# Performance work log

Measured on AMD Instinct MI355X. Metric: run time of the kernel, lower is better.

The kernel has to match this reference:

```python
import jax, jax.numpy as jnp
import numpy as np

N, F, C1, H, C2, E = 50000, 256, 32, 8, 16, 800000
NEG_SLOPE = 0.2


def gat_layer(x, src, dst, W, a_src, a_dst, b, heads, out_c, concat):
    n = x.shape[0]
    h = (x @ W).reshape(n, heads, out_c)               # [N,H,C]
    al_src = jnp.sum(h * a_src, axis=-1)               # [N,H]
    al_dst = jnp.sum(h * a_dst, axis=-1)               # [N,H]
    e = jax.nn.leaky_relu(al_src[src] + al_dst[dst], NEG_SLOPE)  # [E,H]
    # segment softmax over incoming edges of each dst node
    m = jax.ops.segment_max(e, dst, num_segments=n)
    e = jnp.exp(e - m[dst])
    denom = jax.ops.segment_sum(e, dst, num_segments=n)
    alpha = e / (denom[dst] + 1e-16)                   # [E,H]
    msg = h[src] * alpha[..., None]                    # [E,H,C]
    out = jax.ops.segment_sum(msg, dst, num_segments=n)
    out = out.reshape(n, heads * out_c) if concat else out.mean(axis=1)
    return out + b


def conv1d(x, w, b):
    # x: [1,C,N], w: [O,I,K], 'same' padding (K=5 -> pad 2)
    pad = (w.shape[-1] - 1) // 2
    y = jax.lax.conv_general_dilated(x, w, (1,), [(pad, pad)],
                                     dimension_numbers=('NCH', 'OIH', 'NCH'))
    return y + b[None, :, None]


def setup_inputs() -> dict:
    key = jax.random.key(0)
    ks = jax.random.split(key, 20)
    s = lambda k, shp, sc: jax.random.normal(k, shp, jnp.float32) * sc
    inp = {
        'x': jax.random.normal(ks[0], (N, F), jnp.float32),
        'edge_index': jax.random.randint(ks[1], (2, E), 0, N, jnp.int32),
        'W1': s(ks[2], (F, H * C1), 0.06),
        'a_src1': s(ks[3], (H, C1), 0.1), 'a_dst1': s(ks[4], (H, C1), 0.1),
        'b1': jnp.zeros((H * C1,), jnp.float32),
        'W2': s(ks[5], (H * C1, C2), 0.06),
        'a_src2': s(ks[6], (1, C2), 0.1), 'a_dst2': s(ks[7], (1, C2), 0.1),
        'b2': jnp.zeros((C2,), jnp.float32),
        'proj_w': s(ks[8], (C2, 1), 0.2), 'proj_b': jnp.zeros((1,), jnp.float32),
        'c1_w': s(ks[9], (C2, C2, 5), 0.1), 'c1_b': jnp.zeros((C2,), jnp.float32),
        'c2_w': s(ks[10], (C2, C2, 5), 0.1), 'c2_b': jnp.zeros((C2,), jnp.float32),
        'lin_w': s(ks[11], (2 * C2, C2), 0.15), 'lin_b': jnp.zeros((C2,), jnp.float32),
    }
    return inp


def reference(x, edge_index, W1, a_src1, a_dst1, b1, W2, a_src2, a_dst2, b2,
              proj_w, proj_b, c1_w, c1_b, c2_w, c2_b, lin_w, lin_b):
    n = x.shape[0]
    loops = jnp.arange(n, dtype=edge_index.dtype)
    src = jnp.concatenate([edge_index[0], loops])  # PyG GATConv adds self-loops
    dst = jnp.concatenate([edge_index[1], loops])

    h = jax.nn.relu(gat_layer(x, src, dst, W1, a_src1, a_dst1, b1, H, C1, True))
    x1 = gat_layer(h, src, dst, W2, a_src2, a_dst2, b2, 1, C2, False)  # [N,C2]

    g = (x1 @ proj_w + proj_b)[:, 0]                  # [N]
    sort_idx = jnp.argsort(g)
    inverse_idx = jnp.argsort(sort_idx)
    sorted_x = g[sort_idx][:, None] * x1[sort_idx]    # [N,C2]
    sx = sorted_x.T[None]                             # [1,C2,N]
    sx = jax.nn.relu(conv1d(sx, c1_w, c1_b))
    sx = conv1d(sx, c2_w, c2_b)
    x2 = sx[0].T[inverse_idx]                         # [N,C2]

    out = jnp.concatenate([x1, x2], axis=1) @ lin_w + lin_b
    return jax.nn.log_softmax(out, axis=1)
```

## Files before the change

### kernel.cpp

```cpp
#include <hip/hip_runtime.h>
#include <math.h>

#define NBUCKET 65536

__device__ __forceinline__ float leakyrelu02(float v) { return v > 0.f ? v : 0.2f * v; }

__global__ __launch_bounds__(256) void k_gemm1(const float* __restrict__ A,
                                               const float* __restrict__ B,
                                               float* __restrict__ C, int M) {
  __shared__ float As[16][132];
  __shared__ float Bs[16][68];
  const int m0 = blockIdx.x * 128;
  const int n0 = blockIdx.y * 64;
  const int tid = threadIdx.x;
  const int tm = tid & 15;
  const int tn = tid >> 4;
  float acc[8][4];
#pragma unroll
  for (int i = 0; i < 8; ++i)
#pragma unroll
    for (int j = 0; j < 4; ++j) acc[i][j] = 0.f;

  const int ar = tid & 127, aseg = (tid >> 7) * 8;
  const int br = tid >> 4, bc = (tid & 15) * 4;

  for (int k0 = 0; k0 < 256; k0 += 16) {
    float4 a0 = make_float4(0.f, 0.f, 0.f, 0.f);
    float4 a1 = make_float4(0.f, 0.f, 0.f, 0.f);
    if (m0 + ar < M) {
      const float* ap = A + (size_t)(m0 + ar) * 256 + k0 + aseg;
      a0 = *(const float4*)(ap);
      a1 = *(const float4*)(ap + 4);
    }
    As[aseg + 0][ar] = a0.x;
    As[aseg + 1][ar] = a0.y;
    As[aseg + 2][ar] = a0.z;
    As[aseg + 3][ar] = a0.w;
    As[aseg + 4][ar] = a1.x;
    As[aseg + 5][ar] = a1.y;
    As[aseg + 6][ar] = a1.z;
    As[aseg + 7][ar] = a1.w;
    *(float4*)&Bs[br][bc] = *(const float4*)(B + (size_t)(k0 + br) * 256 + n0 + bc);
    __syncthreads();
#pragma unroll
    for (int kk = 0; kk < 16; ++kk) {
      float a[8], b[4];
      *(float4*)&a[0] = *(const float4*)&As[kk][tm * 4];
      *(float4*)&a[4] = *(const float4*)&As[kk][64 + tm * 4];
      *(float4*)&b[0] = *(const float4*)&Bs[kk][tn * 4];
#pragma unroll
      for (int i = 0; i < 8; ++i)
#pragma unroll
        for (int j = 0; j < 4; ++j) acc[i][j] += a[i] * b[j];
    }
    __syncthreads();
  }
#pragma unroll
  for (int i = 0; i < 8; ++i) {
    int m = m0 + ((i < 4) ? (tm * 4 + i) : (64 + tm * 4 + i - 4));
    if (m < M) {
      float4 o = make_float4(acc[i][0], acc[i][1], acc[i][2], acc[i][3]);
      *(float4*)(C + (size_t)m * 256 + n0 + tn * 4) = o;
    }
  }
}

__global__ __launch_bounds__(256) void k_al1(const float* __restrict__ h_lin,
                                             const float* __restrict__ a_src,
                                             const float* __restrict__ a_dst,
                                             float* __restrict__ als,
                                             float* __restrict__ ald, int N) {
  int gid = blockIdx.x * 256 + threadIdx.x;
  int n = gid >> 6;
  int l = threadIdx.x & 63;
  if (n >= N) return;
  float4 h4 = *(const float4*)(h_lin + (size_t)n * 256 + l * 4);
  float4 vs = *(const float4*)(a_src + l * 4);
  float4 vd = *(const float4*)(a_dst + l * 4);
  float ps = h4.x * vs.x + h4.y * vs.y + h4.z * vs.z + h4.w * vs.w;
  float pd = h4.x * vd.x + h4.y * vd.y + h4.z * vd.z + h4.w * vd.w;
  ps += __shfl_xor(ps, 1); pd += __shfl_xor(pd, 1);
  ps += __shfl_xor(ps, 2); pd += __shfl_xor(pd, 2);
  ps += __shfl_xor(ps, 4); pd += __shfl_xor(pd, 4);
  if ((l & 7) == 0) {
    als[(size_t)n * 8 + (l >> 3)] = ps;
    ald[(size_t)n * 8 + (l >> 3)] = pd;
  }
}

__global__ __launch_bounds__(256) void k_hist(const int* __restrict__ ei,
                                              int* __restrict__ counts, int E, int N) {
  int e = blockIdx.x * 256 + threadIdx.x;
  if (e >= E + N) return;
  int d = (e < E) ? ei[E + e] : (e - E);
  atomicAdd(&counts[d], 1);
}

__global__ __launch_bounds__(1024) void k_scan(const int* __restrict__ counts,
                                               int* __restrict__ offsets,
                                               int* __restrict__ cursor, int chunk) {
  __shared__ int part[1024];
  const int t = threadIdx.x;
  const int base = t * chunk;
  int ssum = 0;
  for (int i = 0; i < chunk; i += 4) {
    int4 v = *(const int4*)(counts + base + i);
    ssum += v.x + v.y + v.z + v.w;
  }
  part[t] = ssum;
  __syncthreads();
  for (int d = 1; d < 1024; d <<= 1) {
    int v = (t >= d) ? part[t - d] : 0;
    __syncthreads();
    part[t] += v;
    __syncthreads();
  }
  int run = (t == 0) ? 0 : part[t - 1];
  for (int i = 0; i < chunk; i += 4) {
    int4 v = *(const int4*)(counts + base + i);
    int4 o;
    o.x = run; run += v.x;
    o.y = run; run += v.y;
    o.z = run; run += v.z;
    o.w = run; run += v.w;
    *(int4*)(offsets + base + i) = o;
    if (cursor) *(int4*)(cursor + base + i) = o;
  }
  if (t == 1023) offsets[1024 * chunk] = run;
}

__global__ __launch_bounds__(256) void k_scatter_ew(
    const int* __restrict__ ei, const float* __restrict__ als1,
    const float* __restrict__ ald1, int* __restrict__ cursor,
    int* __restrict__ csr_src, int* __restrict__ csr_dst,
    float* __restrict__ ew, int E, int N) {
  int e = blockIdx.x * 256 + threadIdx.x;
  if (e >= E + N) return;
  int d, s;
  if (e < E) { d = ei[E + e]; s = ei[e]; }
  else { d = e - E; s = d; }
  int pos = atomicAdd(&cursor[d], 1);
  csr_src[pos] = s;
  csr_dst[pos] = d;
  float4 as0 = *(const float4*)(als1 + (size_t)s * 8);
  float4 as1 = *(const float4*)(als1 + (size_t)s * 8 + 4);
  float4 ad0 = *(const float4*)(ald1 + (size_t)d * 8);
  float4 ad1 = *(const float4*)(ald1 + (size_t)d * 8 + 4);
  float4 w0, w1;
  w0.x = expf(leakyrelu02(as0.x + ad0.x));
  w0.y = expf(leakyrelu02(as0.y + ad0.y));
  w0.z = expf(leakyrelu02(as0.z + ad0.z));
  w0.w = expf(leakyrelu02(as0.w + ad0.w));
  w1.x = expf(leakyrelu02(as1.x + ad1.x));
  w1.y = expf(leakyrelu02(as1.y + ad1.y));
  w1.z = expf(leakyrelu02(as1.z + ad1.z));
  w1.w = expf(leakyrelu02(as1.w + ad1.w));
  *(float4*)(ew + (size_t)pos * 8) = w0;
  *(float4*)(ew + (size_t)pos * 8 + 4) = w1;
}

__global__ __launch_bounds__(256) void k_ew2(const int* __restrict__ csr_src,
                                             const int* __restrict__ csr_dst,
                                             const float* __restrict__ als2,
                                             const float* __restrict__ ald2,
                                             float* __restrict__ ew2, int Etot) {
  int t = blockIdx.x * 256 + threadIdx.x;
  if (t >= Etot) return;
  ew2[t] = expf(leakyrelu02(als2[csr_src[t]] + ald2[csr_dst[t]]));
}

__global__ __launch_bounds__(256) void k_gat1(
    const float* __restrict__ h_lin, const float* __restrict__ ew,
    const float* __restrict__ b1, const int* __restrict__ offsets,
    const int* __restrict__ csr_src, const float* __restrict__ W2,
    const float* __restrict__ a_src2, const float* __restrict__ a_dst2,
    float* __restrict__ h2, float* __restrict__ als2, float* __restrict__ ald2, int N) {
  __shared__ float w2s[4352];
  __shared__ float rowbuf[4][256];
  for (int i = threadIdx.x; i < 4096; i += 256) w2s[(i >> 4) * 17 + (i & 15)] = W2[i];
  __syncthreads();

  const int w = threadIdx.x >> 6;
  const int l = threadIdx.x & 63;
  const int half = l >> 5;
  const int li = l & 31;
  const int h3 = li >> 2;
  const int n = blockIdx.x * 4 + w;
  if (n >= N) return;

  const int off = offsets[n];
  const int deg = offsets[n + 1] - off;
  const float* hb = h_lin + li * 8;

  float c0 = 0.f, c1 = 0.f, c2 = 0.f, c3 = 0.f, c4 = 0.f, c5 = 0.f, c6 = 0.f, c7 = 0.f;
  float sw = 0.f;
  int e = 0;
  for (; e + 8 <= deg; e += 8) {
    const int p0 = off + e + half;
    int s0 = csr_src[p0];
    int s1 = csr_src[p0 + 2];
    int s2 = csr_src[p0 + 4];
    int s3 = csr_src[p0 + 6];
    float w0 = ew[(size_t)p0 * 8 + h3];
    float w1 = ew[(size_t)(p0 + 2) * 8 + h3];
    float w2v = ew[(size_t)(p0 + 4) * 8 + h3];
    float w3 = ew[(size_t)(p0 + 6) * 8 + h3];
    const float* r0p = hb + (size_t)s0 * 256;
    const float* r1p = hb + (size_t)s1 * 256;
    const float* r2p = hb + (size_t)s2 * 256;
    const float* r3p = hb + (size_t)s3 * 256;
    float4 r0a = *(const float4*)(r0p), r0b = *(const float4*)(r0p + 4);
    float4 r1a = *(const float4*)(r1p), r1b = *(const float4*)(r1p + 4);
    float4 r2a = *(const float4*)(r2p), r2b = *(const float4*)(r2p + 4);
    float4 r3a = *(const float4*)(r3p), r3b = *(const float4*)(r3p + 4);
    sw += (w0 + w1) + (w2v + w3);
    c0 += w0 * r0a.x + w1 * r1a.x + w2v * r2a.x + w3 * r3a.x;
    c1 += w0 * r0a.y + w1 * r1a.y + w2v * r2a.y + w3 * r3a.y;
    c2 += w0 * r0a.z + w1 * r1a.z + w2v * r2a.z + w3 * r3a.z;
    c3 += w0 * r0a.w + w1 * r1a.w + w2v * r2a.w + w3 * r3a.w;
    c4 += w0 * r0b.x + w1 * r1b.x + w2v * r2b.x + w3 * r3b.x;
    c5 += w0 * r0b.y + w1 * r1b.y + w2v * r2b.y + w3 * r3b.y;
    c6 += w0 * r0b.z + w1 * r1b.z + w2v * r2b.z + w3 * r3b.z;
    c7 += w0 * r0b.w + w1 * r1b.w + w2v * r2b.w + w3 * r3b.w;
  }
  for (; e < deg; e += 2) {
    int ee = e + half;
    if (ee < deg) {
      int p = off + ee;
      int s = csr_src[p];
      float ww = ew[(size_t)p * 8 + h3];
      const float* rp = hb + (size_t)s * 256;
      float4 ra = *(const float4*)(rp), rb = *(const float4*)(rp + 4);
      sw += ww;
      c0 += ww * ra.x; c1 += ww * ra.y; c2 += ww * ra.z; c3 += ww * ra.w;
      c4 += ww * rb.x; c5 += ww * rb.y; c6 += ww * rb.z; c7 += ww * rb.w;
    }
  }
  c0 += __shfl_xor(c0, 32); c1 += __shfl_xor(c1, 32);
  c2 += __shfl_xor(c2, 32); c3 += __shfl_xor(c3, 32);
  c4 += __shfl_xor(c4, 32); c5 += __shfl_xor(c5, 32);
  c6 += __shfl_xor(c6, 32); c7 += __shfl_xor(c7, 32);
  sw += __shfl_xor(sw, 32);
  const float inv = 1.f / (sw + 1e-16f);

  if (half == 0) {
    float4 ba = *(const float4*)(b1 + li * 8);
    float4 bbv = *(const float4*)(b1 + li * 8 + 4);
    rowbuf[w][li * 8 + 0] = fmaxf(c0 * inv + ba.x, 0.f);
    rowbuf[w][li * 8 + 1] = fmaxf(c1 * inv + ba.y, 0.f);
    rowbuf[w][li * 8 + 2] = fmaxf(c2 * inv + ba.z, 0.f);
    rowbuf[w][li * 8 + 3] = fmaxf(c3 * inv + ba.w, 0.f);
    rowbuf[w][li * 8 + 4] = fmaxf(c4 * inv + bbv.x, 0.f);
    rowbuf[w][li * 8 + 5] = fmaxf(c5 * inv + bbv.y, 0.f);
    rowbuf[w][li * 8 + 6] = fmaxf(c6 * inv + bbv.z, 0.f);
    rowbuf[w][li * 8 + 7] = fmaxf(c7 * inv + bbv.w, 0.f);
  }
  asm volatile("s_waitcnt lgkmcnt(0)" ::: "memory");

  const int o = l & 15;
  const int grp = l >> 4;
  float a2 = 0.f;
#pragma unroll 8
  for (int t = 0; t < 64; ++t) {
    int cc = grp * 64 + ((t + grp * 8) & 63);
    a2 += rowbuf[w][cc] * w2s[cc * 17 + o];
  }
  a2 += __shfl_xor(a2, 16);
  a2 += __shfl_xor(a2, 32);

  if (l < 16) {
    h2[(size_t)n * 16 + l] = a2;
    float ps = a2 * a_src2[l];
    float pd = a2 * a_dst2[l];
    ps += __shfl_xor(ps, 1); pd += __shfl_xor(pd, 1);
    ps += __shfl_xor(ps, 2); pd += __shfl_xor(pd, 2);
    ps += __shfl_xor(ps, 4); pd += __shfl_xor(pd, 4);
    ps += __shfl_xor(ps, 8); pd += __shfl_xor(pd, 8);
    if (l == 0) { als2[n] = ps; ald2[n] = pd; }
  }
}

__global__ __launch_bounds__(256) void k_gat2(
    const float* __restrict__ h2, const float* __restrict__ ew2,
    const float* __restrict__ b2, const float* __restrict__ proj_w,
    const float* __restrict__ proj_b, const int* __restrict__ offsets,
    const int* __restrict__ csr_src, float* __restrict__ x1,
    float* __restrict__ g, unsigned long long* __restrict__ keys,
    int* __restrict__ bhist, int N) {
  const int w = threadIdx.x >> 6;
  const int l = threadIdx.x & 63;
  const int n = blockIdx.x * 4 + w;
  if (n >= N) return;
  const int off = offsets[n];
  const int deg = offsets[n + 1] - off;
  const int slot = l >> 4;
  const int c = l & 15;

  float acc = 0.f, sw = 0.f;
  int e0 = 0;
  for (; e0 + 8 <= deg; e0 += 8) {
    int pA = off + e0 + slot;
    int pB = off + e0 + 4 + slot;
    int sA = csr_src[pA];
    int sB = csr_src[pB];
    float wA = ew2[pA];
    float wB = ew2[pB];
    float hA = h2[(size_t)sA * 16 + c];
    float hB = h2[(size_t)sB * 16 + c];
    sw += wA + wB;
    acc += wA * hA + wB * hB;
  }
  for (; e0 < deg; e0 += 4) {
    int e = e0 + slot;
    if (e < deg) {
      int p = off + e;
      int s = csr_src[p];
      float v = ew2[p];
      sw += v;
      acc += v * h2[(size_t)s * 16 + c];
    }
  }
  acc += __shfl_xor(acc, 16); sw += __shfl_xor(sw, 16);
  acc += __shfl_xor(acc, 32); sw += __shfl_xor(sw, 32);
  float x1v = acc / (sw + 1e-16f) + b2[c];

  float pg = x1v * proj_w[c];
  pg += __shfl_xor(pg, 1);
  pg += __shfl_xor(pg, 2);
  pg += __shfl_xor(pg, 4);
  pg += __shfl_xor(pg, 8);
  if (l < 16) x1[(size_t)n * 16 + l] = x1v;
  if (l == 0) {
    float gv = pg + proj_b[0];
    g[n] = gv;
    unsigned u = __float_as_uint(gv);
    u = (u & 0x80000000u) ? ~u : (u | 0x80000000u);
    keys[n] = (((unsigned long long)u) << 32) | (unsigned)n;
    atomicAdd(&bhist[u >> 16], 1);
  }
}

__global__ __launch_bounds__(256) void k_bscatter(const unsigned long long* __restrict__ keys,
                                                  int* __restrict__ cursor,
                                                  unsigned long long* __restrict__ bkeys, int N) {
  int n = blockIdx.x * 256 + threadIdx.x;
  if (n >= N) return;
  unsigned long long k = keys[n];
  int b = (int)(k >> 48);
  int pos = atomicAdd(&cursor[b], 1);
  bkeys[pos] = k;
}

__global__ __launch_bounds__(256) void k_brank(const unsigned long long* __restrict__ bkeys,
                                               const int* __restrict__ boffs,
                                               const float* __restrict__ g,
                                               const float* __restrict__ x1,
                                               int* __restrict__ rank,
                                               float* __restrict__ sortedv, int N) {
  int pos = blockIdx.x * 256 + threadIdx.x;
  if (pos >= N) return;
  unsigned long long k = bkeys[pos];
  int b = (int)(k >> 48);
  int lo = boffs[b], hi = boffs[b + 1];
  int r = lo;
  for (int j = lo; j < hi; ++j) r += (bkeys[j] < k) ? 1 : 0;
  int idx = (int)(unsigned)(k & 0xffffffffull);
  rank[idx] = r;
  float gv = g[idx];
#pragma unroll
  for (int c = 0; c < 16; c += 4) {
    float4 v = *(const float4*)(x1 + (size_t)idx * 16 + c);
    float4 o = make_float4(gv * v.x, gv * v.y, gv * v.z, gv * v.w);
    *(float4*)(sortedv + (size_t)r * 16 + c) = o;
  }
}

__global__ __launch_bounds__(256) void k_conv(const float* __restrict__ in,
                                              const float* __restrict__ wgt,
                                              const float* __restrict__ bias,
                                              float* __restrict__ out, int N, int relu) {
  __shared__ float s[260][17];
  __shared__ float ws[1280];
  __shared__ float bs[16];
  const int p0 = blockIdx.x * 256;
  for (int i = threadIdx.x; i < 1280; i += 256) ws[i] = wgt[i];
  if (threadIdx.x < 16) bs[threadIdx.x] = bias[threadIdx.x];
  for (int idx = threadIdx.x; idx < 260 * 16; idx += 256) {
    int lp = idx >> 4, c = idx & 15;
    int gp = p0 - 2 + lp;
    s[lp][c] = (gp >= 0 && gp < N) ? in[(size_t)gp * 16 + c] : 0.f;
  }
  __syncthreads();
  const int p = p0 + threadIdx.x;
  if (p >= N) return;
  float acc[16];
#pragma unroll
  for (int o = 0; o < 16; ++o) acc[o] = bs[o];
  for (int k = 0; k < 5; ++k) {
    for (int c = 0; c < 16; ++c) {
      float xv = s[threadIdx.x + k][c];
#pragma unroll
      for (int o = 0; o < 16; ++o) acc[o] += ws[(o * 16 + c) * 5 + k] * xv;
    }
  }
#pragma unroll
  for (int o = 0; o < 16; ++o) {
    float v = acc[o];
    if (relu) v = fmaxf(v, 0.f);
    out[(size_t)p * 16 + o] = v;
  }
}

__global__ __launch_bounds__(256) void k_final(
    const float* __restrict__ x1, const float* __restrict__ c2out,
    const int* __restrict__ rank, const float* __restrict__ lin_w,
    const float* __restrict__ lin_b, float* __restrict__ out, int N) {
  __shared__ float lw[512];
  __shared__ float lb[16];
  for (int i = threadIdx.x; i < 512; i += 256) lw[i] = lin_w[i];
  if (threadIdx.x < 16) lb[threadIdx.x] = lin_b[threadIdx.x];
  __syncthreads();
  const int n = blockIdx.x * 256 + threadIdx.x;
  if (n >= N) return;
  float xa[16], xb[16];
  const int r = rank[n];
#pragma unroll
  for (int c = 0; c < 16; c += 4) {
    float4 va = *(const float4*)(x1 + (size_t)n * 16 + c);
    float4 vb = *(const float4*)(c2out + (size_t)r * 16 + c);
    xa[c] = va.x; xa[c + 1] = va.y; xa[c + 2] = va.z; xa[c + 3] = va.w;
    xb[c] = vb.x; xb[c + 1] = vb.y; xb[c + 2] = vb.z; xb[c + 3] = vb.w;
  }
  float z[16];
#pragma unroll
  for (int o = 0; o < 16; ++o) z[o] = lb[o];
#pragma unroll
  for (int c = 0; c < 16; ++c) {
    float va = xa[c], vb = xb[c];
#pragma unroll
    for (int o = 0; o < 16; ++o) z[o] += va * lw[c * 16 + o] + vb * lw[(16 + c) * 16 + o];
  }
  float m = z[0];
#pragma unroll
  for (int o = 1; o < 16; ++o) m = fmaxf(m, z[o]);
  float ssum = 0.f;
#pragma unroll
  for (int o = 0; o < 16; ++o) ssum += expf(z[o] - m);
  float lse = m + logf(ssum);
#pragma unroll
  for (int o = 0; o < 16; ++o) out[(size_t)n * 16 + o] = z[o] - lse;
}

extern "C" void kernel_launch(void* const* d_in, const int* in_sizes, int n_in,
                              void* d_out, int out_size, void* d_ws, size_t ws_size,
                              hipStream_t stream) {
  const float* x = (const float*)d_in[0];
  const int* ei = (const int*)d_in[1];
  const float* W1 = (const float*)d_in[2];
  const float* a_src1 = (const float*)d_in[3];
  const float* a_dst1 = (const float*)d_in[4];
  const float* b1 = (const float*)d_in[5];
  const float* W2 = (const float*)d_in[6];
  const float* a_src2 = (const float*)d_in[7];
  const float* a_dst2 = (const float*)d_in[8];
  const float* b2 = (const float*)d_in[9];
  const float* proj_w = (const float*)d_in[10];
  const float* proj_b = (const float*)d_in[11];
  const float* c1_w = (const float*)d_in[12];
  const float* c1_b = (const float*)d_in[13];
  const float* c2_w = (const float*)d_in[14];
  const float* c2_b = (const float*)d_in[15];
  const float* lin_w = (const float*)d_in[16];
  const float* lin_b = (const float*)d_in[17];
  float* out = (float*)d_out;

  const int N = in_sizes[0] / 256;
  const int E = in_sizes[1] / 2;
  const int Etot = E + N;

  int chunk = (N + 1023) / 1024;
  chunk = (chunk + 3) & ~3;
  const int Npad = 1024 * chunk;

  char* ws = (char*)d_ws;
  size_t off = 0;
  auto alloc = [&](size_t bytes) -> void* {
    void* p = ws + off;
    off = (off + bytes + 255) & ~(size_t)255;
    return p;
  };
  float* h_lin = (float*)alloc((size_t)N * 256 * 4);
  float* als1 = (float*)alloc((size_t)N * 8 * 4);
  float* ald1 = (float*)alloc((size_t)N * 8 * 4);
  int* counts = (int*)alloc((size_t)Npad * 4);
  int* offsets = (int*)alloc((size_t)(Npad + 1) * 4);
  int* cursor = (int*)alloc((size_t)Npad * 4);
  int* csr_src = (int*)alloc((size_t)Etot * 4);
  int* csr_dst = (int*)alloc((size_t)Etot * 4);
  float* ew = (float*)alloc((size_t)Etot * 8 * 4);
  float* ew2 = (float*)alloc((size_t)Etot * 4);
  float* h2 = (float*)alloc((size_t)N * 16 * 4);
  float* als2 = (float*)alloc((size_t)N * 4);
  float* ald2 = (float*)alloc((size_t)N * 4);
  float* x1 = (float*)alloc((size_t)N * 16 * 4);
  float* gbuf = (float*)alloc((size_t)N * 4);
  unsigned long long* keys = (unsigned long long*)alloc((size_t)N * 8);
  int* bhist = (int*)alloc((size_t)NBUCKET * 4);
  int* boffs = (int*)alloc((size_t)(NBUCKET + 1) * 4);
  int* bcursor = (int*)alloc((size_t)NBUCKET * 4);
  unsigned long long* bkeys = (unsigned long long*)alloc((size_t)N * 8);
  int* rank = (int*)alloc((size_t)N * 4);
  float* sortedv = (float*)alloc((size_t)N * 16 * 4);
  float* c1out = (float*)alloc((size_t)N * 16 * 4);
  float* c2out = (float*)alloc((size_t)N * 16 * 4);
  if (off > ws_size) return;

  hipMemsetAsync(counts, 0, (size_t)Npad * 4, stream);
  hipMemsetAsync(bhist, 0, (size_t)NBUCKET * 4, stream);

  dim3 gg((N + 127) / 128, 4);
  k_gemm1<<<gg, 256, 0, stream>>>(x, W1, h_lin, N);
  k_al1<<<(N + 3) / 4, 256, 0, stream>>>(h_lin, a_src1, a_dst1, als1, ald1, N);
  k_hist<<<(Etot + 255) / 256, 256, 0, stream>>>(ei, counts, E, N);
  k_scan<<<1, 1024, 0, stream>>>(counts, offsets, cursor, chunk);
  k_scatter_ew<<<(Etot + 255) / 256, 256, 0, stream>>>(ei, als1, ald1, cursor,
                                                       csr_src, csr_dst, ew, E, N);
  k_gat1<<<(N + 3) / 4, 256, 0, stream>>>(h_lin, ew, b1, offsets, csr_src,
                                          W2, a_src2, a_dst2, h2, als2, ald2, N);
  k_ew2<<<(Etot + 255) / 256, 256, 0, stream>>>(csr_src, csr_dst, als2, ald2, ew2, Etot);
  k_gat2<<<(N + 3) / 4, 256, 0, stream>>>(h2, ew2, b2, proj_w, proj_b,
                                          offsets, csr_src, x1, gbuf, keys, bhist, N);
  k_scan<<<1, 1024, 0, stream>>>(bhist, boffs, bcursor, NBUCKET / 1024);
  k_bscatter<<<(N + 255) / 256, 256, 0, stream>>>(keys, bcursor, bkeys, N);
  k_brank<<<(N + 255) / 256, 256, 0, stream>>>(bkeys, boffs, gbuf, x1, rank, sortedv, N);
  k_conv<<<(N + 255) / 256, 256, 0, stream>>>(sortedv, c1_w, c1_b, c1out, N, 1);
  k_conv<<<(N + 255) / 256, 256, 0, stream>>>(c1out, c2_w, c2_b, c2out, N, 0);
  k_final<<<(N + 255) / 256, 256, 0, stream>>>(x1, c2out, rank, lin_w, lin_b, out, N);
}
```

Measured before the change: 552.0 us.

## Widen GEMM tile to 128x128 and read W2 from global in gat1

The first GEMM now computes a 128x128 output tile per block with an 8x8 register accumulator per thread, which halves the grid's y-dimension and reuses each A tile across twice as many columns. In k_gat1, the per-block shared-memory staging of W2 and its block-wide barrier are removed. W2 is read directly from global memory (cached), and rowbuf gets padding to reduce LDS bank conflicts. The cost is higher register pressure in the GEMM and more global/cache traffic for W2 in the GAT kernel.

After: 597.5 us. 1.08x slower.

```diff
diff --git a/kernel.cpp b/kernel.cpp
--- a/kernel.cpp
+++ b/kernel.cpp
@@ -9,20 +9,20 @@
                                                const float* __restrict__ B,
                                                float* __restrict__ C, int M) {
   __shared__ float As[16][132];
-  __shared__ float Bs[16][68];
+  __shared__ float Bs[16][132];
   const int m0 = blockIdx.x * 128;
-  const int n0 = blockIdx.y * 64;
+  const int n0 = blockIdx.y * 128;
   const int tid = threadIdx.x;
   const int tm = tid & 15;
   const int tn = tid >> 4;
-  float acc[8][4];
+  float acc[8][8];
 #pragma unroll
   for (int i = 0; i < 8; ++i)
 #pragma unroll
-    for (int j = 0; j < 4; ++j) acc[i][j] = 0.f;
+    for (int j = 0; j < 8; ++j) acc[i][j] = 0.f;
 
   const int ar = tid & 127, aseg = (tid >> 7) * 8;
-  const int br = tid >> 4, bc = (tid & 15) * 4;
+  const int br = tid >> 4, bc = (tid & 15) * 8;
 
   for (int k0 = 0; k0 < 256; k0 += 16) {
     float4 a0 = make_float4(0.f, 0.f, 0.f, 0.f);
@@ -40,18 +40,21 @@
     As[aseg + 5][ar] = a1.y;
     As[aseg + 6][ar] = a1.z;
     As[aseg + 7][ar] = a1.w;
-    *(float4*)&Bs[br][bc] = *(const float4*)(B + (size_t)(k0 + br) * 256 + n0 + bc);
+    const float* bp = B + (size_t)(k0 + br) * 256 + n0 + bc;
+    *(float4*)&Bs[br][bc] = *(const float4*)(bp);
+    *(float4*)&Bs[br][bc + 4] = *(const float4*)(bp + 4);
     __syncthreads();
 #pragma unroll
     for (int kk = 0; kk < 16; ++kk) {
-      float a[8], b[4];
+      float a[8], b[8];
       *(float4*)&a[0] = *(const float4*)&As[kk][tm * 4];
       *(float4*)&a[4] = *(const float4*)&As[kk][64 + tm * 4];
       *(float4*)&b[0] = *(const float4*)&Bs[kk][tn * 4];
+      *(float4*)&b[4] = *(const float4*)&Bs[kk][64 + tn * 4];
 #pragma unroll
       for (int i = 0; i < 8; ++i)
 #pragma unroll
-        for (int j = 0; j < 4; ++j) acc[i][j] += a[i] * b[j];
+        for (int j = 0; j < 8; ++j) acc[i][j] += a[i] * b[j];
     }
     __syncthreads();
   }
@@ -59,8 +62,10 @@
   for (int i = 0; i < 8; ++i) {
     int m = m0 + ((i < 4) ? (tm * 4 + i) : (64 + tm * 4 + i - 4));
     if (m < M) {
-      float4 o = make_float4(acc[i][0], acc[i][1], acc[i][2], acc[i][3]);
-      *(float4*)(C + (size_t)m * 256 + n0 + tn * 4) = o;
+      float4 o0 = make_float4(acc[i][0], acc[i][1], acc[i][2], acc[i][3]);
+      float4 o1 = make_float4(acc[i][4], acc[i][5], acc[i][6], acc[i][7]);
+      *(float4*)(C + (size_t)m * 256 + n0 + tn * 4) = o0;
+      *(float4*)(C + (size_t)m * 256 + n0 + 64 + tn * 4) = o1;
     }
   }
 }
@@ -169,16 +174,15 @@
   ew2[t] = expf(leakyrelu02(als2[csr_src[t]] + ald2[csr_dst[t]]));
 }
 
+#define RB(i) ((i) + ((i) >> 3))
+
 __global__ __launch_bounds__(256) void k_gat1(
     const float* __restrict__ h_lin, const float* __restrict__ ew,
     const float* __restrict__ b1, const int* __restrict__ offsets,
     const int* __restrict__ csr_src, const float* __restrict__ W2,
     const float* __restrict__ a_src2, const float* __restrict__ a_dst2,
     float* __restrict__ h2, float* __restrict__ als2, float* __restrict__ ald2, int N) {
-  __shared__ float w2s[4352];
-  __shared__ float rowbuf[4][256];
-  for (int i = threadIdx.x; i < 4096; i += 256) w2s[(i >> 4) * 17 + (i & 15)] = W2[i];
-  __syncthreads();
+  __shared__ float rowbuf[4][292];
 
   const int w = threadIdx.x >> 6;
   const int l = threadIdx.x & 63;
@@ -246,14 +250,14 @@
   if (half == 0) {
     float4 ba = *(const float4*)(b1 + li * 8);
     float4 bbv = *(const float4*)(b1 + li * 8 + 4);
-    rowbuf[w][li * 8 + 0] = fmaxf(c0 * inv + ba.x, 0.f);
-    rowbuf[w][li * 8 + 1] = fmaxf(c1 * inv + ba.y, 0.f);
-    rowbuf[w][li * 8 + 2] = fmaxf(c2 * inv + ba.z, 0.f);
-    rowbuf[w][li * 8 + 3] = fmaxf(c3 * inv + ba.w, 0.f);
-    rowbuf[w][li * 8 + 4] = fmaxf(c4 * inv + bbv.x, 0.f);
-    rowbuf[w][li * 8 + 5] = fmaxf(c5 * inv + bbv.y, 0.f);
-    rowbuf[w][li * 8 + 6] = fmaxf(c6 * inv + bbv.z, 0.f);
-    rowbuf[w][li * 8 + 7] = fmaxf(c7 * inv + bbv.w, 0.f);
+    rowbuf[w][RB(li * 8 + 0)] = fmaxf(c0 * inv + ba.x, 0.f);
+    rowbuf[w][RB(li * 8 + 1)] = fmaxf(c1 * inv + ba.y, 0.f);
+    rowbuf[w][RB(li * 8 + 2)] = fmaxf(c2 * inv + ba.z, 0.f);
+    rowbuf[w][RB(li * 8 + 3)] = fmaxf(c3 * inv + ba.w, 0.f);
+    rowbuf[w][RB(li * 8 + 4)] = fmaxf(c4 * inv + bbv.x, 0.f);
+    rowbuf[w][RB(li * 8 + 5)] = fmaxf(c5 * inv + bbv.y, 0.f);
+    rowbuf[w][RB(li * 8 + 6)] = fmaxf(c6 * inv + bbv.z, 0.f);
+    rowbuf[w][RB(li * 8 + 7)] = fmaxf(c7 * inv + bbv.w, 0.f);
   }
   asm volatile("s_waitcnt lgkmcnt(0)" ::: "memory");
 
@@ -263,7 +267,7 @@
 #pragma unroll 8
   for (int t = 0; t < 64; ++t) {
     int cc = grp * 64 + ((t + grp * 8) & 63);
-    a2 += rowbuf[w][cc] * w2s[cc * 17 + o];
+    a2 += rowbuf[w][RB(cc)] * W2[cc * 16 + o];
   }
   a2 += __shfl_xor(a2, 16);
   a2 += __shfl_xor(a2, 32);
@@ -518,7 +522,7 @@
   hipMemsetAsync(counts, 0, (size_t)Npad * 4, stream);
   hipMemsetAsync(bhist, 0, (size_t)NBUCKET * 4, stream);
 
-  dim3 gg((N + 127) / 128, 4);
+  dim3 gg((N + 127) / 128, 2);
   k_gemm1<<<gg, 256, 0, stream>>>(x, W1, h_lin, N);
   k_al1<<<(N + 3) / 4, 256, 0, stream>>>(h_lin, a_src1, a_dst1, als1, ald1, N);
   k_hist<<<(Etot + 255) / 256, 256, 0, stream>>>(ei, counts, E, N);
```
